# Optimization experiments

Measured on AMD Instinct MI355X. Metric: run time of the kernel, lower is better.

The kernel has to match this reference:

```python
import jax, jax.numpy as jnp
import numpy as np

B, N, K = 2, 4096, 16
CIN, CQ, D, PH, AH = 128, 128, 256, 64, 1024  # AH = dim * attn_hidden_multiplier
EPS = 1e-5


def setup_inputs() -> dict:
    key = jax.random.key(0)
    ks = jax.random.split(key, 40)
    rn = lambda k, shape, s=0.05: (jax.random.normal(k, shape, jnp.float32) * s)
    inp = {
        'obj_feature': jax.random.normal(ks[0], (B, CIN, N), jnp.float32),
        'pos': jax.random.normal(ks[1], (B, 3, N), jnp.float32),
        'query_points': jax.random.normal(ks[2], (B, CQ, N), jnp.float32),
        # linear_start_query / linear_start_obj (1x1 Conv1d)
        'W_lsq': rn(ks[3], (D, CQ)), 'b_lsq': rn(ks[4], (D,)),
        'W_lso': rn(ks[5], (D, CIN)), 'b_lso': rn(ks[6], (D,)),
        # key / query / value 1x1 Conv1d
        'Wk': rn(ks[7], (D, D)), 'bk': rn(ks[8], (D,)),
        'Wq': rn(ks[9], (D, D)), 'bq': rn(ks[10], (D,)),
        'Wv': rn(ks[11], (D, D)), 'bv': rn(ks[12], (D,)),
        # pos_mlp: Conv2d(3,PH,1) -> BN -> ReLU -> Conv2d(PH,D,1)
        'Wp1': rn(ks[13], (PH, 3)), 'bp1': rn(ks[14], (PH,)),
        'g1': 1.0 + rn(ks[15], (PH,)), 'bt1': rn(ks[16], (PH,)),
        'm1': rn(ks[17], (PH,)), 'v1': 0.5 + jax.random.uniform(ks[18], (PH,), jnp.float32),
        'Wp2': rn(ks[19], (D, PH)), 'bp2': rn(ks[20], (D,)),
        # attn_mlp: Conv2d(D,AH,1) -> BN -> ReLU -> Conv2d(AH,D,1)
        'Wa1': rn(ks[21], (AH, D)), 'ba1': rn(ks[22], (AH,)),
        'g2': 1.0 + rn(ks[23], (AH,)), 'bt2': rn(ks[24], (AH,)),
        'm2': rn(ks[25], (AH,)), 'v2': 0.5 + jax.random.uniform(ks[26], (AH,), jnp.float32),
        'Wa2': rn(ks[27], (D, AH)), 'ba2': rn(ks[28], (D,)),
        # linear_end
        'We': rn(ks[29], (CIN, D)), 'bfin': rn(ks[30], (CIN,)),
    }
    return inp


def _conv1d(x, W, b):  # x: (B,Ci,N), W: (Co,Ci)
    return jnp.einsum('oi,bin->bon', W, x) + b[None, :, None]


def _conv2d(x, W, b):  # x: (B,Ci,N,K)
    return jnp.einsum('oi,bink->bonk', W, x) + b[None, :, None, None]


def _bn(x, g, bt, m, v):  # inference BatchNorm2d over channel axis 1
    sc = (g * jax.lax.rsqrt(v + EPS))[None, :, None, None]
    return x * sc + (bt - m * g * jax.lax.rsqrt(v + EPS))[None, :, None, None]


def _knn_idx(pos):  # pos: (B,3,N) -> (B,N,K) indices of K nearest points (incl. self)
    p = jnp.transpose(pos, (0, 2, 1))  # (B,N,3)
    sq = jnp.sum(p * p, axis=-1)  # (B,N)
    dist = sq[:, :, None] + sq[:, None, :] - 2.0 * jnp.einsum('bnd,bmd->bnm', p, p)
    return jax.lax.top_k(-dist, K)[1]


def _gather(feat, idx):  # feat: (B,C,N), idx: (B,N,K) -> (B,C,N,K)
    return jnp.take_along_axis(feat[:, :, None, :], idx[:, None, :, :], axis=3)


def reference(obj_feature, pos, query_points, W_lsq, b_lsq, W_lso, b_lso,
              Wk, bk, Wq, bq, Wv, bv, Wp1, bp1, g1, bt1, m1, v1, Wp2, bp2,
              Wa1, ba1, g2, bt2, m2, v2, Wa2, ba2, We, bfin):
    qf = _conv1d(query_points, W_lsq, b_lsq)        # (B,D,N)
    of = _conv1d(obj_feature, W_lso, b_lso)         # (B,D,N)
    idx = _knn_idx(pos)                             # (B,N,K)
    key = _conv1d(of, Wk, bk)
    value = _conv1d(of, Wv, bv)
    query = _conv1d(qf, Wq, bq)
    key_g = _gather(key, idx)                       # (B,D,N,K)
    qk_rel = query[:, :, :, None] - key_g
    pos_rel = pos[:, :, :, None] - _gather(pos, idx)  # (B,3,N,K)
    pe = _conv2d(jax.nn.relu(_bn(_conv2d(pos_rel, Wp1, bp1), g1, bt1, m1, v1)), Wp2, bp2)
    attn = _conv2d(jax.nn.relu(_bn(_conv2d(qk_rel + pe, Wa1, ba1), g2, bt2, m2, v2)), Wa2, ba2)
    attn = jax.nn.softmax(attn, axis=-1)            # softmax over K neighbors
    val = value[:, :, :, None] + pe                 # (B,D,N,K)
    agg = jnp.sum(attn * val, axis=-1)              # einsum 'bcij,bcij->bci'
    return _conv1d(agg, We, bfin)                   # (B,CIN,N)
```

## Files before the change

kernel.cpp:

```cpp
#include <hip/hip_runtime.h>
#include <stdint.h>

#define B_ 2
#define N_ 4096
#define KNN 16
#define D_ 256
#define EPS_ 1e-5f
#define COLS_TOTAL (B_ * N_ * KNN)
#define LOGNCHK 3

typedef unsigned short u16;
typedef unsigned long long u64;
typedef __bf16 bf16x8 __attribute__((ext_vector_type(8)));
typedef float f32x4 __attribute__((ext_vector_type(4)));

__device__ __forceinline__ float bu2f(u16 u) { return __uint_as_float(((unsigned)u) << 16); }
__device__ __forceinline__ u16 f2bu(float f) {
  __bf16 h = (__bf16)f;
  return __builtin_bit_cast(unsigned short, h);
}
__device__ __forceinline__ float rdl(const void* p, size_t i, int f) {
  return f ? bu2f(((const u16*)p)[i]) : ((const float*)p)[i];
}

#define SC_POS 0
#define SC_BLSQ 24576
#define SC_BLSO 24832
#define SC_BK 25088
#define SC_BQ 25344
#define SC_BV 25600
#define SC_WP1 25856
#define SC_BP1 26048
#define SC_G1 26112
#define SC_BT1 26176
#define SC_M1 26240
#define SC_V1 26304
#define SC_BP2 26368
#define SC_BA1 26624
#define SC_G2 27648
#define SC_BT2 28672
#define SC_M2 29696
#define SC_V2 30720
#define SC_BA2 31744
#define SC_BFIN 32000
#define SC_BQP 32128
#define SC_BKP 32384
#define SC_BVP 32640
#define SC_W1S 32896
#define SC_C1  33088
#define SC_ASC 33152
#define SC_ASH 34176
#define SC_TOT 35200

#define NSEG 29
struct Seg { const void* s; float* d; int n; };
struct SegTab { Seg seg[NSEG]; };
__global__ void ingest(SegTab t, const unsigned* __restrict__ praw,
                       int* __restrict__ flagp, int total) {
  __shared__ int cnt;
  if (threadIdx.x == 0) cnt = 0;
  __syncthreads();
  unsigned wv = praw[threadIdx.x];
  unsigned e = (wv >> 7) & 0xFFu;
  if (e >= 0x7Au && e <= 0x81u) atomicAdd(&cnt, 1);
  __syncthreads();
  int f = (cnt >= 128) ? 1 : 0;
  if (blockIdx.x == 0 && threadIdx.x == 0) *flagp = f;
  int tid = blockIdx.x * blockDim.x + threadIdx.x;
  if (tid >= total) return;
  int acc = 0, k = 0;
  for (k = 0; k < NSEG; k++) { if (tid < acc + t.seg[k].n) break; acc += t.seg[k].n; }
  int i = tid - acc;
  t.seg[k].d[i] = rdl(t.seg[k].s, i, f);
}

__device__ void dev_bnprep(float* scal, int t) {
  if (t < 1024) {
    float sc = scal[SC_G2 + t] * (1.0f / sqrtf(scal[SC_V2 + t] + EPS_));
    scal[SC_ASC + t] = sc;
    scal[SC_ASH + t] = scal[SC_BA1 + t] * sc + (scal[SC_BT2 + t] - scal[SC_M2 + t] * sc);
  }
  if (t < 64) {
    float sc1 = scal[SC_G1 + t] * (1.0f / sqrtf(scal[SC_V1 + t] + EPS_));
    scal[SC_C1 + t] = scal[SC_BP1 + t] * sc1 + (scal[SC_BT1 + t] - scal[SC_M1 + t] * sc1);
    for (int i = 0; i < 3; i++) scal[SC_W1S + t * 3 + i] = scal[SC_WP1 + t * 3 + i] * sc1;
  }
}

struct C3 { const float* Wo[3]; const float* Wi[3]; const float* bi[3]; const float* bo[3];
            u16* Wout[3]; float* bout[3]; };
__device__ void dev_compose3(const C3& c, int z, int tid) {
  const float* Wo = c.Wo[z]; const float* Wi = c.Wi[z];
  if (tid < 256 * 128) {
    int o = tid >> 7, i = tid & 127;
    float a0 = 0.f, a1 = 0.f, a2 = 0.f, a3 = 0.f;
    for (int d = 0; d < 256; d += 4) {
      a0 += Wo[o * 256 + d + 0] * Wi[(d + 0) * 128 + i];
      a1 += Wo[o * 256 + d + 1] * Wi[(d + 1) * 128 + i];
      a2 += Wo[o * 256 + d + 2] * Wi[(d + 2) * 128 + i];
      a3 += Wo[o * 256 + d + 3] * Wi[(d + 3) * 128 + i];
    }
    c.Wout[z][o * 128 + i] = f2bu((a0 + a1) + (a2 + a3));
  } else if (tid < 256 * 128 + 256) {
    int o = tid - 256 * 128;
    float a = c.bo[z][o];
    for (int d = 0; d < 256; d++) a += Wo[o * 256 + d] * c.bi[z][d];
    c.bout[z][o] = a;
  }
}

struct QF { const float* src[3]; u16* dst[3]; int M[3]; int K[3]; };
__device__ void dev_quant_flin(const QF& q, int z, int g) {
  int M = q.M[z], K = q.K[z];
  if (g >= (M * K) / 8) return;
  int tile = g >> 6, lane = g & 63;
  int l15 = lane & 15, quad = lane >> 4;
  int kt = K >> 5;
  int mt = tile / kt, kc = tile % kt;
  const float* s = q.src[z] + (size_t)(mt * 16 + l15) * K + kc * 32 + quad * 8;
  u16* d = q.dst[z] + (size_t)g * 8;
  u16 o[8];
#pragma unroll
  for (int j = 0; j < 8; j++) o[j] = f2bu(s[j]);
  *(uint4*)d = *(uint4*)o;
}

struct T2 { const void* src[2]; u16* dst[2]; };
__device__ void dev_transq2(const T2& t2, int f, int bx, int by, int bz, int tid,
                            u16 (*t)[33]) {
  int tensor = bz >> 1, b = bz & 1;
  const void* raw = t2.src[tensor];
  u16* out = t2.dst[tensor];
  int c0 = by * 32, n0 = bx * 32;
  int j = tid & 31, i0 = tid >> 5;
  for (int s = 0; s < 32; s += 8) {
    int i = i0 + s;
    t[i][j] = f2bu(rdl(raw, ((size_t)b * 128 + c0 + i) * N_ + n0 + j, f));
  }
  __syncthreads();
  int i = tid & 31, j0 = tid >> 5;
  for (int s = 0; s < 32; s += 8) {
    int jj = j0 + s;
    out[((size_t)b * N_ + n0 + jj) * 128 + c0 + i] = t[i][jj];
  }
}

__device__ __forceinline__ u64 knn_key(const float* px, float qx, float qy, float qz,
                                       float sqn, int m) {
  float cx = px[m], cy = px[N_ + m], cz = px[2 * N_ + m];
  float sqm = cx * cx + cy * cy + cz * cz;
  float dot = qx * cx + qy * cy + qz * cz;
  float d = (sqn + sqm) - 2.0f * dot;
  unsigned ub = __float_as_uint(d);
  ub = ((int)ub < 0) ? ~ub : (ub | 0x80000000u);
  return ((u64)ub << 32) | (unsigned)m;
}

__device__ __forceinline__ void bitonic_sort16(u64* c) {
#pragma unroll
  for (int k = 2; k <= 16; k <<= 1) {
#pragma unroll
    for (int j = k >> 1; j > 0; j >>= 1) {
#pragma unroll
      for (int i = 0; i < 16; i++) {
        int l = i ^ j;
        if (l > i) {
          u64 a = c[i], b2 = c[l];
          bool up = ((i & k) == 0);
          bool sw = up ? (b2 < a) : (a < b2);
          u64 na = sw ? b2 : a;
          u64 nb = sw ? a : b2;
          c[i] = na; c[l] = nb;
        }
      }
    }
  }
}

__device__ __forceinline__ void bitonic_merge_into(u64* best, const u64* c) {
#pragma unroll
  for (int i = 0; i < 16; i++) {
    u64 b2 = c[15 - i];
    best[i] = (best[i] < b2) ? best[i] : b2;
  }
#pragma unroll
  for (int j = 8; j > 0; j >>= 1) {
#pragma unroll
    for (int i = 0; i < 16; i++) {
      if ((i & j) == 0) {
        u64 a = best[i], b2 = best[i | j];
        u64 mn = (a < b2) ? a : b2;
        u64 mx = (a < b2) ? b2 : a;
        best[i] = mn; best[i | j] = mx;
      }
    }
  }
}

__device__ void dev_knn_partial(const float* pos, u64* part, int tid) {
  int n = tid & (N_ - 1);
  int ch = (tid >> 12) & ((1 << LOGNCHK) - 1);
  int b = tid >> (12 + LOGNCHK);
  const float* px = pos + (size_t)b * 3 * N_;
  float qx = px[n], qy = px[N_ + n], qz = px[2 * N_ + n];
  float sqn = qx * qx + qy * qy + qz * qz;
  int clen = N_ >> LOGNCHK;
  int m0 = ch * clen;
  u64 best[KNN];
  {
#pragma unroll
    for (int i = 0; i < 16; i++) best[i] = knn_key(px, qx, qy, qz, sqn, m0 + i);
    bitonic_sort16(best);
  }
  for (int m = m0 + 16; m < m0 + clen; m += 16) {
    u64 c[16];
#pragma unroll
    for (int i = 0; i < 16; i++) c[i] = knn_key(px, qx, qy, qz, sqn, m + i);
    bitonic_sort16(c);
    bitonic_merge_into(best, c);
  }
  u64* o = part + (size_t)tid * KNN;
#pragma unroll
  for (int i = 0; i < KNN; i++) o[i] = best[i];
}

__device__ void dev_knn_merge(const u64* part, int* idx, int tid) {
  if (tid >= B_ * N_) return;
  int n = tid & (N_ - 1);
  int b = tid >> 12;
  u64 best[KNN];
  {
    const u64* p = part + ((((size_t)(b << LOGNCHK)) << 12) + n) * KNN;
#pragma unroll
    for (int i = 0; i < KNN; i++) best[i] = p[i];
  }
  for (int ch = 1; ch < (1 << LOGNCHK); ch++) {
    const u64* p = part + ((((size_t)((b << LOGNCHK) + ch)) << 12) + n) * KNN;
    u64 c[16];
#pragma unroll
    for (int e = 0; e < KNN; e++) c[e] = p[e];
    bitonic_merge_into(best, c);
  }
  int* o = idx + (size_t)tid * KNN;
#pragma unroll
  for (int i = 0; i < KNN; i++) o[i] = (int)(best[i] & 0xffffffffu);
}

struct G3 { const u16* W[3]; const u16* Bsrc[3]; u16* O[3]; const float* bias[3]; };
__device__ void dev_gemm(const G3& g, int bx, int by, int bz, int tid,
                         u16* As, u16* Bs) {
  const int z = bz;
  const u16* Wg = g.W[z];
  const u16* Bg = g.Bsrc[z];
  u16* Out = g.O[z];
  const float* bias = g.bias[z];
  const int M = 256, K = 128;
  const int mtile = by, ctile = bx;
  const int wid = tid >> 6, lane = tid & 63;
  const int wm = wid >> 1, wc = wid & 1;
  const int l15 = lane & 15, quad = lane >> 4;
  f32x4 acc[4][4];
#pragma unroll
  for (int a = 0; a < 4; a++)
#pragma unroll
    for (int bb = 0; bb < 4; bb++) acc[a][bb] = (f32x4){0.f, 0.f, 0.f, 0.f};
  const int r0 = tid >> 2, q0 = tid & 3;
  for (int k0 = 0; k0 < K; k0 += 32) {
    __syncthreads();
    *(uint4*)(&As[(r0) * 32 + q0 * 8]) = *(const uint4*)(&Wg[((size_t)mtile * 128 + r0) * K + k0 + q0 * 8]);
    *(uint4*)(&As[(r0 + 64) * 32 + q0 * 8]) = *(const uint4*)(&Wg[((size_t)mtile * 128 + r0 + 64) * K + k0 + q0 * 8]);
    *(uint4*)(&Bs[(r0) * 32 + q0 * 8]) = *(const uint4*)(&Bg[((size_t)ctile * 128 + r0) * K + k0 + q0 * 8]);
    *(uint4*)(&Bs[(r0 + 64) * 32 + q0 * 8]) = *(const uint4*)(&Bg[((size_t)ctile * 128 + r0 + 64) * K + k0 + q0 * 8]);
    __syncthreads();
    bf16x8 af[4], bfr[4];
#pragma unroll
    for (int i = 0; i < 4; i++) {
      af[i] = *(const bf16x8*)(&As[(wm * 64 + i * 16 + l15) * 32 + quad * 8]);
      bfr[i] = *(const bf16x8*)(&Bs[(wc * 64 + i * 16 + l15) * 32 + quad * 8]);
    }
#pragma unroll
    for (int mi = 0; mi < 4; mi++)
#pragma unroll
      for (int ni = 0; ni < 4; ni++)
        acc[mi][ni] = __builtin_amdgcn_mfma_f32_16x16x32_bf16(af[mi], bfr[ni], acc[mi][ni], 0, 0, 0);
  }
  const int mbase = mtile * 128 + wm * 64;
  const int cbase = ctile * 128 + wc * 64;
#pragma unroll
  for (int mi = 0; mi < 4; mi++) {
#pragma unroll
    for (int ni = 0; ni < 4; ni++) {
      int m0 = mbase + mi * 16 + quad * 4;
      int c = cbase + ni * 16 + l15;
      u16 pk[4];
#pragma unroll
      for (int r = 0; r < 4; r++) pk[r] = f2bu(acc[mi][ni][r] + bias[m0 + r]);
      *(uint2*)(&Out[(size_t)c * M + m0]) = *(uint2*)pk;
    }
  }
}

__global__ void prepA(C3 c3, QF qf, T2 t2, float* __restrict__ scal,
                      u64* __restrict__ knn_part, const int* __restrict__ flagp) {
  __shared__ u16 tq[32][33];
  int bid = blockIdx.x, tid = threadIdx.x;
  if (bid < 256) {
    dev_knn_partial(scal + SC_POS, knn_part, bid * 256 + tid);
  } else if (bid < 260) {
    dev_bnprep(scal, (bid - 256) * 256 + tid);
  } else if (bid < 650) {
    int u = bid - 260;
    dev_compose3(c3, u / 130, (u % 130) * 256 + tid);
  } else if (bid < 1034) {
    int u = bid - 650;
    dev_quant_flin(qf, u >> 7, (u & 127) * 256 + tid);
  } else {
    int u = bid - 1034;
    dev_transq2(t2, *flagp, u & 127, (u >> 7) & 3, u >> 9, tid, tq);
  }
}

__global__ __launch_bounds__(256) void prepB(G3 g3, const u64* __restrict__ knn_part,
                                             int* __restrict__ idx) {
  __shared__ __align__(16) u16 As[128 * 32];
  __shared__ __align__(16) u16 Bs[128 * 32];
  int bid = blockIdx.x, tid = threadIdx.x;
  if (bid < 32) {
    dev_knn_merge(knn_part, idx, bid * 256 + tid);
  } else {
    int u = bid - 32;
    dev_gemm(g3, u & 63, (u >> 6) & 1, u >> 7, tid, As, Bs);
  }
}

#define XS_OFF 0
#define HS_OFF 16896
#define AG_OFF 33792
#define SM_TOT 35872

__global__ __launch_bounds__(512, 4) void mega(
    const float* __restrict__ scal, const int* __restrict__ idx,
    const u16* __restrict__ query_t, const u16* __restrict__ key_t,
    const u16* __restrict__ value_t,
    float* __restrict__ out,
    const u16* __restrict__ Wp2f, const u16* __restrict__ Wa1f,
    const u16* __restrict__ Wa2f, const float* __restrict__ Wef) {
  __shared__ __align__(16) u16 sm[SM_TOT];
  float* aggs = (float*)&sm[AG_OFF];
  const int tid = threadIdx.x;
  const int w = tid >> 6, lane = tid & 63;
  const int l15 = lane & 15, quad = lane >> 4;
  const int gcol0 = blockIdx.x * 64;
  const int b = gcol0 >> 16;
  const int n0 = (gcol0 & 65535) >> 4;

  uint4 qu_r[4], ku_r[4];
  {
#pragma unroll
    for (int it = 0; it < 4; it++) {
      int g = tid + it * 512;
      int col = g >> 5, dg = (g & 31) * 8;
      int n = n0 + (col >> 4), k = col & 15;
      int id = idx[((size_t)(b * N_ + n)) * KNN + k];
      qu_r[it] = *(const uint4*)(query_t + ((size_t)(b * N_ + n)) * D_ + dg);
      ku_r[it] = *(const uint4*)(key_t + ((size_t)(b * N_ + id)) * D_ + dg);
    }
  }

  {
    int col = tid >> 3, jg = (tid & 7) * 8;
    int n = n0 + (col >> 4), k = col & 15;
    int id = idx[((size_t)(b * N_ + n)) * KNN + k];
    const float* px = scal + SC_POS + (size_t)b * 3 * N_;
    float pr0 = px[n] - px[id];
    float pr1 = px[N_ + n] - px[N_ + id];
    float pr2 = px[2 * N_ + n] - px[2 * N_ + id];
    u16 o[8];
#pragma unroll
    for (int e = 0; e < 8; e++) {
      int j = jg + e;
      float v = scal[SC_W1S + j * 3] * pr0 + scal[SC_W1S + j * 3 + 1] * pr1 +
                scal[SC_W1S + j * 3 + 2] * pr2 + scal[SC_C1 + j];
      o[e] = f2bu(fmaxf(v, 0.f));
    }
    *(uint4*)(&sm[HS_OFF + col * 264 + jg]) = *(uint4*)o;
  }
  __syncthreads();

  uint2 pe_pk[2][4];
  {
    f32x4 pacc[2][4];
#pragma unroll
    for (int mi = 0; mi < 2; mi++)
#pragma unroll
      for (int ni = 0; ni < 4; ni++) pacc[mi][ni] = (f32x4){0.f, 0.f, 0.f, 0.f};
    __builtin_amdgcn_s_setprio(1);
#pragma unroll
    for (int kc = 0; kc < 2; kc++) {
      int k0 = kc * 32;
      bf16x8 af[2], bfr[4];
#pragma unroll
      for (int mi = 0; mi < 2; mi++)
        af[mi] = *(const bf16x8*)(Wp2f + (size_t)((w * 2 + mi) * 2 + kc) * 512 + lane * 8);
#pragma unroll
      for (int ni = 0; ni < 4; ni++)
        bfr[ni] = *(const bf16x8*)(&sm[HS_OFF + (ni * 16 + l15) * 264 + k0 + quad * 8]);
#pragma unroll
      for (int mi = 0; mi < 2; mi++)
#pragma unroll
        for (int ni = 0; ni < 4; ni++)
          pacc[mi][ni] = __builtin_amdgcn_mfma_f32_16x16x32_bf16(af[mi], bfr[ni], pacc[mi][ni], 0, 0, 0);
    }
    __builtin_amdgcn_s_setprio(0);
#pragma unroll
    for (int mi = 0; mi < 2; mi++)
#pragma unroll
      for (int ni = 0; ni < 4; ni++) {
        int m0 = w * 32 + mi * 16 + quad * 4;
        int col = ni * 16 + l15;
        u16 pk[4];
#pragma unroll
        for (int r = 0; r < 4; r++) pk[r] = f2bu(pacc[mi][ni][r] + scal[SC_BP2 + m0 + r]);
        uint2 pu = *(uint2*)pk;
        pe_pk[mi][ni] = pu;
        *(uint2*)(&sm[XS_OFF + col * 264 + m0]) = pu;
      }
  }
  __syncthreads();

  {
    uint4 xbuf[4];
#pragma unroll
    for (int it = 0; it < 4; it++) {
      int g = tid + it * 512;
      int col = g >> 5, dg = (g & 31) * 8;
      uint4 pu = *(const uint4*)(&sm[XS_OFF + col * 264 + dg]);
      const u16 *qs = (const u16*)&qu_r[it], *ks = (const u16*)&ku_r[it], *ps = (const u16*)&pu;
      u16 o[8];
#pragma unroll
      for (int e = 0; e < 8; e++) o[e] = f2bu((bu2f(qs[e]) - bu2f(ks[e])) + bu2f(ps[e]));
      xbuf[it] = *(uint4*)o;
    }
    __syncthreads();
#pragma unroll
    for (int it = 0; it < 4; it++) {
      int g = tid + it * 512;
      int col = g >> 5, dg = (g & 31) * 8;
      *(uint4*)(&sm[XS_OFF + col * 264 + dg]) = xbuf[it];
    }
  }
  __syncthreads();

  f32x4 aacc[2][4];
#pragma unroll
  for (int mi = 0; mi < 2; mi++)
#pragma unroll
    for (int ni = 0; ni < 4; ni++) aacc[mi][ni] = (f32x4){0.f, 0.f, 0.f, 0.f};

  for (int hb = 0; hb < 4; hb++) {
    f32x4 hacc[2][4];
#pragma unroll
    for (int mi = 0; mi < 2; mi++)
#pragma unroll
      for (int ni = 0; ni < 4; ni++) hacc[mi][ni] = (f32x4){0.f, 0.f, 0.f, 0.f};
    __builtin_amdgcn_s_setprio(1);
#pragma unroll 4
    for (int kc = 0; kc < 8; kc++) {
      int k0 = kc * 32;
      bf16x8 af[2], bx[4];
#pragma unroll
      for (int mi = 0; mi < 2; mi++)
        af[mi] = *(const bf16x8*)(Wa1f + (size_t)((hb * 16 + w * 2 + mi) * 8 + kc) * 512 + lane * 8);
#pragma unroll
      for (int ni = 0; ni < 4; ni++)
        bx[ni] = *(const bf16x8*)(&sm[XS_OFF + (ni * 16 + l15) * 264 + k0 + quad * 8]);
#pragma unroll
      for (int mi = 0; mi < 2; mi++)
#pragma unroll
        for (int ni = 0; ni < 4; ni++)
          hacc[mi][ni] = __builtin_amdgcn_mfma_f32_16x16x32_bf16(af[mi], bx[ni], hacc[mi][ni], 0, 0, 0);
    }
    __builtin_amdgcn_s_setprio(0);
    __syncthreads();
#pragma unroll
    for (int mi = 0; mi < 2; mi++)
#pragma unroll
      for (int ni = 0; ni < 4; ni++) {
        int khb = w * 32 + mi * 16 + quad * 4;
        int mh = hb * 256 + khb;
        int col = ni * 16 + l15;
        u16 pk[4];
#pragma unroll
        for (int r = 0; r < 4; r++) {
          float v = hacc[mi][ni][r] * scal[SC_ASC + mh + r] + scal[SC_ASH + mh + r];
          pk[r] = f2bu(fmaxf(v, 0.f));
        }
        *(uint2*)(&sm[HS_OFF + col * 264 + khb]) = *(uint2*)pk;
      }
    __syncthreads();
    __builtin_amdgcn_s_setprio(1);
#pragma unroll 4
    for (int kc = 0; kc < 8; kc++) {
      int k0 = kc * 32;
      bf16x8 af[2], bh[4];
#pragma unroll
      for (int mi = 0; mi < 2; mi++)
        af[mi] = *(const bf16x8*)(Wa2f + (size_t)((w * 2 + mi) * 32 + hb * 8 + kc) * 512 + lane * 8);
#pragma unroll
      for (int ni = 0; ni < 4; ni++)
        bh[ni] = *(const bf16x8*)(&sm[HS_OFF + (ni * 16 + l15) * 264 + k0 + quad * 8]);
#pragma unroll
      for (int mi = 0; mi < 2; mi++)
#pragma unroll
        for (int ni = 0; ni < 4; ni++)
          aacc[mi][ni] = __builtin_amdgcn_mfma_f32_16x16x32_bf16(af[mi], bh[ni], aacc[mi][ni], 0, 0, 0);
    }
    __builtin_amdgcn_s_setprio(0);
  }

  __syncthreads();
#pragma unroll
  for (int mi = 0; mi < 2; mi++)
#pragma unroll
    for (int ni = 0; ni < 4; ni++) {
      int m0 = w * 32 + mi * 16 + quad * 4;
      int col = ni * 16 + l15;
      u16 pk[4];
#pragma unroll
      for (int r = 0; r < 4; r++) pk[r] = f2bu(aacc[mi][ni][r] + scal[SC_BA2 + m0 + r]);
      *(uint2*)(&sm[XS_OFF + col * 264 + m0]) = *(uint2*)pk;
      *(uint2*)(&sm[HS_OFF + col * 264 + m0]) = pe_pk[mi][ni];
    }
  __syncthreads();

#pragma unroll
  for (int it = 0; it < 2; it++) {
    int e = tid + it * 512;
    int pt = e >> 8, m = e & 255;
    float a[16];
#pragma unroll
    for (int k = 0; k < 16; k++) a[k] = bu2f(sm[XS_OFF + (pt * 16 + k) * 264 + m]);
    float t0 = fmaxf(a[0], a[1]),  t1 = fmaxf(a[2], a[3]);
    float t2 = fmaxf(a[4], a[5]),  t3 = fmaxf(a[6], a[7]);
    float t4 = fmaxf(a[8], a[9]),  t5 = fmaxf(a[10], a[11]);
    float t6 = fmaxf(a[12], a[13]), t7 = fmaxf(a[14], a[15]);
    t0 = fmaxf(t0, t1); t2 = fmaxf(t2, t3); t4 = fmaxf(t4, t5); t6 = fmaxf(t6, t7);
    float mx = fmaxf(fmaxf(t0, t2), fmaxf(t4, t6));
    float s = 0.f;
#pragma unroll
    for (int k = 0; k < 16; k++) { a[k] = __expf(a[k] - mx); s += a[k]; }
    float inv = __builtin_amdgcn_rcpf(s);
    float acc = 0.f;
#pragma unroll
    for (int k = 0; k < 16; k++)
      acc += a[k] * bu2f(sm[HS_OFF + (pt * 16 + k) * 264 + m]);
    float val = bu2f(value_t[((size_t)(b * N_ + n0 + pt)) * D_ + m]);
    aggs[pt * 260 + m] = fmaf(acc, inv, val);
  }
  __syncthreads();

  {
    int ci = tid >> 2, pt = tid & 3;
    float acc = scal[SC_BFIN + ci];
    const float* wr = Wef + (size_t)ci * 256;
    const float* ag = aggs + pt * 260;
#pragma unroll 8
    for (int m4 = 0; m4 < 256; m4 += 4) {
      float4 wu = *(const float4*)(wr + m4);
      acc += wu.x * ag[m4] + wu.y * ag[m4 + 1] + wu.z * ag[m4 + 2] + wu.w * ag[m4 + 3];
    }
    out[((size_t)(b * 128 + ci)) * N_ + n0 + pt] = acc;
  }
}

#define WT_LSQ 0
#define WT_LSO 32768
#define WT_K 65536
#define WT_Q 131072
#define WT_V 196608
#define WT_P2 262144
#define WT_A1 278528
#define WT_A2 540672
#define WT_TOT 802816
#define WB_QP 0
#define WB_KP 32768
#define WB_VP 65536
#define WB_P2 98304
#define WB_A1 114688
#define WB_A2 376832
#define WB_TOT 638976

extern "C" void kernel_launch(void* const* d_in, const int* in_sizes, int n_in,
                              void* d_out, int out_size, void* d_ws, size_t ws_size,
                              hipStream_t stream) {
  (void)in_sizes; (void)n_in; (void)out_size; (void)ws_size;
  char* wsb = (char*)d_ws;
  size_t off = 0;
  auto alloc = [&](size_t bytes) -> void* {
    void* p = wsb + off;
    off = (off + bytes + 255) & ~(size_t)255;
    return p;
  };
  int* flag = (int*)alloc(256);
  int* idx = (int*)alloc((size_t)B_ * N_ * KNN * 4);
  u16* wbf = (u16*)alloc((size_t)WB_TOT * 2);
  float* scal = (float*)alloc((size_t)SC_TOT * 4);
  float* Wef = (float*)alloc((size_t)32768 * 4);
  u16* key_t = (u16*)alloc((size_t)B_ * N_ * D_ * 2);
  u16* query_t = (u16*)alloc((size_t)B_ * N_ * D_ * 2);
  u16* value_t = (u16*)alloc((size_t)B_ * N_ * D_ * 2);
  float* wtmp = (float*)alloc((size_t)WT_TOT * 4);
  u16* qp_t = (u16*)alloc((size_t)B_ * N_ * 128 * 2);
  u16* obj_t = (u16*)alloc((size_t)B_ * N_ * 128 * 2);
  u64* knn_part = (u64*)alloc(((size_t)(B_ * N_) << LOGNCHK) * KNN * 8);

  SegTab st;
  int si = 0;
  auto seg = [&](int di, float* d, int n) { st.seg[si].s = d_in[di]; st.seg[si].d = d; st.seg[si].n = n; si++; };
  seg(1, scal + SC_POS, 24576);
  seg(4, scal + SC_BLSQ, 256); seg(6, scal + SC_BLSO, 256);
  seg(8, scal + SC_BK, 256); seg(10, scal + SC_BQ, 256); seg(12, scal + SC_BV, 256);
  seg(13, scal + SC_WP1, 192); seg(14, scal + SC_BP1, 64); seg(15, scal + SC_G1, 64);
  seg(16, scal + SC_BT1, 64); seg(17, scal + SC_M1, 64); seg(18, scal + SC_V1, 64);
  seg(20, scal + SC_BP2, 256); seg(22, scal + SC_BA1, 1024);
  seg(23, scal + SC_G2, 1024); seg(24, scal + SC_BT2, 1024); seg(25, scal + SC_M2, 1024);
  seg(26, scal + SC_V2, 1024); seg(28, scal + SC_BA2, 256); seg(30, scal + SC_BFIN, 128);
  seg(3, wtmp + WT_LSQ, 32768); seg(5, wtmp + WT_LSO, 32768);
  seg(7, wtmp + WT_K, 65536); seg(9, wtmp + WT_Q, 65536); seg(11, wtmp + WT_V, 65536);
  seg(19, wtmp + WT_P2, 16384); seg(21, wtmp + WT_A1, 262144);
  seg(27, wtmp + WT_A2, 262144); seg(29, Wef, 32768);
  int total = 32128 + WT_TOT + 32768;
  ingest<<<(total + 255) / 256, 256, 0, stream>>>(st, (const unsigned*)d_in[1], flag, total);

  C3 c3;
  c3.Wo[0] = wtmp + WT_Q; c3.Wi[0] = wtmp + WT_LSQ; c3.bi[0] = scal + SC_BLSQ; c3.bo[0] = scal + SC_BQ;
  c3.Wout[0] = wbf + WB_QP; c3.bout[0] = scal + SC_BQP;
  c3.Wo[1] = wtmp + WT_K; c3.Wi[1] = wtmp + WT_LSO; c3.bi[1] = scal + SC_BLSO; c3.bo[1] = scal + SC_BK;
  c3.Wout[1] = wbf + WB_KP; c3.bout[1] = scal + SC_BKP;
  c3.Wo[2] = wtmp + WT_V; c3.Wi[2] = wtmp + WT_LSO; c3.bi[2] = scal + SC_BLSO; c3.bo[2] = scal + SC_BV;
  c3.Wout[2] = wbf + WB_VP; c3.bout[2] = scal + SC_BVP;
  QF qf;
  qf.src[0] = wtmp + WT_P2; qf.dst[0] = wbf + WB_P2; qf.M[0] = 256;  qf.K[0] = 64;
  qf.src[1] = wtmp + WT_A1; qf.dst[1] = wbf + WB_A1; qf.M[1] = 1024; qf.K[1] = 256;
  qf.src[2] = wtmp + WT_A2; qf.dst[2] = wbf + WB_A2; qf.M[2] = 256;  qf.K[2] = 1024;
  T2 t2;
  t2.src[0] = d_in[2]; t2.dst[0] = qp_t;
  t2.src[1] = d_in[0]; t2.dst[1] = obj_t;
  prepA<<<3082, 256, 0, stream>>>(c3, qf, t2, scal, knn_part, flag);

  G3 g3;
  g3.W[0] = wbf + WB_QP; g3.Bsrc[0] = qp_t;  g3.O[0] = query_t; g3.bias[0] = scal + SC_BQP;
  g3.W[1] = wbf + WB_KP; g3.Bsrc[1] = obj_t; g3.O[1] = key_t;   g3.bias[1] = scal + SC_BKP;
  g3.W[2] = wbf + WB_VP; g3.Bsrc[2] = obj_t; g3.O[2] = value_t; g3.bias[2] = scal + SC_BVP;
  prepB<<<416, 256, 0, stream>>>(g3, knn_part, idx);

  mega<<<COLS_TOTAL / 64, 512, 0, stream>>>(
      scal, idx, query_t, key_t, value_t, (float*)d_out,
      wbf + WB_P2, wbf + WB_A1, wbf + WB_A2, Wef);
}
```

Measured before the change: 380.5 us.

## Fuse qk_rel add into PE epilogue and double KNN partial chunks

The q and k loads now follow the MFMA accumulator layout of the position-encoding GEMM, so the (q - k + pe) sum is computed directly in that epilogue and written to shared memory once. This drops a separate read-modify-write pass over shared memory and two block barriers. Separately, the KNN partial search is split into twice as many chunks (LOGNCHK 3 to 4, 256 to 512 blocks) for more parallelism in prepA, at the cost of more partial results for the merge step to combine. The narrower uint2 global loads may coalesce less well than the previous uint4 loads.

```diff
diff --git a/kernel.cpp b/kernel.cpp
--- a/kernel.cpp
+++ b/kernel.cpp
@@ -7,7 +7,7 @@
 #define D_ 256
 #define EPS_ 1e-5f
 #define COLS_TOTAL (B_ * N_ * KNN)
-#define LOGNCHK 3
+#define LOGNCHK 4
 
 typedef unsigned short u16;
 typedef unsigned long long u64;
@@ -304,18 +304,18 @@
                       u64* __restrict__ knn_part, const int* __restrict__ flagp) {
   __shared__ u16 tq[32][33];
   int bid = blockIdx.x, tid = threadIdx.x;
-  if (bid < 256) {
+  if (bid < 512) {
     dev_knn_partial(scal + SC_POS, knn_part, bid * 256 + tid);
-  } else if (bid < 260) {
-    dev_bnprep(scal, (bid - 256) * 256 + tid);
-  } else if (bid < 650) {
-    int u = bid - 260;
+  } else if (bid < 516) {
+    dev_bnprep(scal, (bid - 512) * 256 + tid);
+  } else if (bid < 906) {
+    int u = bid - 516;
     dev_compose3(c3, u / 130, (u % 130) * 256 + tid);
-  } else if (bid < 1034) {
-    int u = bid - 650;
+  } else if (bid < 1290) {
+    int u = bid - 906;
     dev_quant_flin(qf, u >> 7, (u & 127) * 256 + tid);
   } else {
-    int u = bid - 1034;
+    int u = bid - 1290;
     dev_transq2(t2, *flagp, u & 127, (u >> 7) & 3, u >> 9, tid, tq);
   }
 }
@@ -354,18 +354,22 @@
   const int b = gcol0 >> 16;
   const int n0 = (gcol0 & 65535) >> 4;
 
-  uint4 qu_r[4], ku_r[4];
+  uint2 qr[2][4], kr[2][4];
   {
-#pragma unroll
-    for (int it = 0; it < 4; it++) {
-      int g = tid + it * 512;
-      int col = g >> 5, dg = (g & 31) * 8;
-      int n = n0 + (col >> 4), k = col & 15;
-      int id = idx[((size_t)(b * N_ + n)) * KNN + k];
-      qu_r[it] = *(const uint4*)(query_t + ((size_t)(b * N_ + n)) * D_ + dg);
-      ku_r[it] = *(const uint4*)(key_t + ((size_t)(b * N_ + id)) * D_ + dg);
-    }
-  }
+    int id_c[4];
+#pragma unroll
+    for (int ni = 0; ni < 4; ni++)
+      id_c[ni] = idx[((size_t)(b * N_ + n0 + ni)) * KNN + l15];
+#pragma unroll
+    for (int mi = 0; mi < 2; mi++)
+#pragma unroll
+      for (int ni = 0; ni < 4; ni++) {
+        int m0 = w * 32 + mi * 16 + quad * 4;
+        qr[mi][ni] = *(const uint2*)(query_t + ((size_t)(b * N_ + n0 + ni)) * D_ + m0);
+        kr[mi][ni] = *(const uint2*)(key_t + ((size_t)(b * N_ + id_c[ni])) * D_ + m0);
+      }
+  }
+  __builtin_amdgcn_sched_barrier(0);
 
   {
     int col = tid >> 3, jg = (tid & 7) * 8;
@@ -418,36 +422,18 @@
       for (int ni = 0; ni < 4; ni++) {
         int m0 = w * 32 + mi * 16 + quad * 4;
         int col = ni * 16 + l15;
-        u16 pk[4];
-#pragma unroll
-        for (int r = 0; r < 4; r++) pk[r] = f2bu(pacc[mi][ni][r] + scal[SC_BP2 + m0 + r]);
-        uint2 pu = *(uint2*)pk;
-        pe_pk[mi][ni] = pu;
-        *(uint2*)(&sm[XS_OFF + col * 264 + m0]) = pu;
+        const u16* qs = (const u16*)&qr[mi][ni];
+        const u16* ks = (const u16*)&kr[mi][ni];
+        u16 pkpe[4], pkx[4];
+#pragma unroll
+        for (int r = 0; r < 4; r++) {
+          float pe = pacc[mi][ni][r] + scal[SC_BP2 + m0 + r];
+          pkpe[r] = f2bu(pe);
+          pkx[r] = f2bu(pe + (bu2f(qs[r]) - bu2f(ks[r])));
+        }
+        pe_pk[mi][ni] = *(uint2*)pkpe;
+        *(uint2*)(&sm[XS_OFF + col * 264 + m0]) = *(uint2*)pkx;
       }
-  }
-  __syncthreads();
-
-  {
-    uint4 xbuf[4];
-#pragma unroll
-    for (int it = 0; it < 4; it++) {
-      int g = tid + it * 512;
-      int col = g >> 5, dg = (g & 31) * 8;
-      uint4 pu = *(const uint4*)(&sm[XS_OFF + col * 264 + dg]);
-      const u16 *qs = (const u16*)&qu_r[it], *ks = (const u16*)&ku_r[it], *ps = (const u16*)&pu;
-      u16 o[8];
-#pragma unroll
-      for (int e = 0; e < 8; e++) o[e] = f2bu((bu2f(qs[e]) - bu2f(ks[e])) + bu2f(ps[e]));
-      xbuf[it] = *(uint4*)o;
-    }
-    __syncthreads();
-#pragma unroll
-    for (int it = 0; it < 4; it++) {
-      int g = tid + it * 512;
-      int col = g >> 5, dg = (g & 31) * 8;
-      *(uint4*)(&sm[XS_OFF + col * 264 + dg]) = xbuf[it];
-    }
   }
   __syncthreads();
 
@@ -646,7 +632,7 @@
   T2 t2;
   t2.src[0] = d_in[2]; t2.dst[0] = qp_t;
   t2.src[1] = d_in[0]; t2.dst[1] = obj_t;
-  prepA<<<3082, 256, 0, stream>>>(c3, qf, t2, scal, knn_part, flag);
+  prepA<<<3338, 256, 0, stream>>>(c3, qf, t2, scal, knn_part, flag);
 
   G3 g3;
   g3.W[0] = wbf + WB_QP; g3.Bsrc[0] = qp_t;  g3.O[0] = query_t; g3.bias[0] = scal + SC_BQP;
```

After: 417.5 us. +9.7%, slower.

## Fold ingest kernel into prepA and stage KNN candidates in LDS

Applied to the files above, without the earlier changes.

Removes the separate ingest launch and the fp32 staging buffer. Each prepA block now computes the dtype flag locally and reads raw inputs directly, converting them on the fly inside compose, quantise, BN prep and a smaller canonicalisation step. KNN partials switch to 16 chunks of 256 candidates whose positions are loaded once into shared memory per block, instead of being re-read from global memory. This trades a launch and a global round trip for redundant flag detection in every block and a larger KNN merge stage.

```diff
diff --git a/kernel.cpp b/kernel.cpp
--- a/kernel.cpp
+++ b/kernel.cpp
@@ -7,7 +7,7 @@
 #define D_ 256
 #define EPS_ 1e-5f
 #define COLS_TOTAL (B_ * N_ * KNN)
-#define LOGNCHK 3
+#define LOGNCHK 4
 
 typedef unsigned short u16;
 typedef unsigned long long u64;
@@ -24,104 +24,103 @@
 }
 
 #define SC_POS 0
-#define SC_BLSQ 24576
-#define SC_BLSO 24832
-#define SC_BK 25088
-#define SC_BQ 25344
-#define SC_BV 25600
-#define SC_WP1 25856
-#define SC_BP1 26048
-#define SC_G1 26112
-#define SC_BT1 26176
-#define SC_M1 26240
-#define SC_V1 26304
-#define SC_BP2 26368
-#define SC_BA1 26624
-#define SC_G2 27648
-#define SC_BT2 28672
-#define SC_M2 29696
-#define SC_V2 30720
-#define SC_BA2 31744
-#define SC_BFIN 32000
-#define SC_BQP 32128
-#define SC_BKP 32384
-#define SC_BVP 32640
-#define SC_W1S 32896
-#define SC_C1  33088
-#define SC_ASC 33152
-#define SC_ASH 34176
-#define SC_TOT 35200
-
-#define NSEG 29
+#define SC_BP2 24576
+#define SC_BA2 24832
+#define SC_BFIN 25088
+#define SC_BQP 25216
+#define SC_BKP 25472
+#define SC_BVP 25728
+#define SC_W1S 25984
+#define SC_C1  26176
+#define SC_ASC 26240
+#define SC_ASH 27264
+#define SC_TOT 28288
+
+__device__ int block_flag(const unsigned* __restrict__ praw) {
+  __shared__ int cnt;
+  if (threadIdx.x == 0) cnt = 0;
+  __syncthreads();
+  if (threadIdx.x < 256) {
+    unsigned wv = praw[threadIdx.x];
+    unsigned e = (wv >> 7) & 0xFFu;
+    if (e >= 0x7Au && e <= 0x81u) atomicAdd(&cnt, 1);
+  }
+  __syncthreads();
+  return (cnt >= 128) ? 1 : 0;
+}
+
+#define NSEG 5
 struct Seg { const void* s; float* d; int n; };
 struct SegTab { Seg seg[NSEG]; };
-__global__ void ingest(SegTab t, const unsigned* __restrict__ praw,
-                       int* __restrict__ flagp, int total) {
-  __shared__ int cnt;
-  if (threadIdx.x == 0) cnt = 0;
-  __syncthreads();
-  unsigned wv = praw[threadIdx.x];
-  unsigned e = (wv >> 7) & 0xFFu;
-  if (e >= 0x7Au && e <= 0x81u) atomicAdd(&cnt, 1);
-  __syncthreads();
-  int f = (cnt >= 128) ? 1 : 0;
-  if (blockIdx.x == 0 && threadIdx.x == 0) *flagp = f;
-  int tid = blockIdx.x * blockDim.x + threadIdx.x;
-  if (tid >= total) return;
+#define CANON_TOT 57984
+__device__ void dev_canon(const SegTab& t, int f, int gt) {
+  if (gt >= CANON_TOT) return;
   int acc = 0, k = 0;
-  for (k = 0; k < NSEG; k++) { if (tid < acc + t.seg[k].n) break; acc += t.seg[k].n; }
-  int i = tid - acc;
-  t.seg[k].d[i] = rdl(t.seg[k].s, i, f);
-}
-
-__device__ void dev_bnprep(float* scal, int t) {
+  for (k = 0; k < NSEG; k++) { if (gt < acc + t.seg[k].n) break; acc += t.seg[k].n; }
+  t.seg[k].d[gt - acc] = rdl(t.seg[k].s, gt - acc, f);
+}
+
+struct BN { const void* ba1; const void* g2; const void* bt2; const void* m2; const void* v2;
+            const void* wp1; const void* bp1; const void* g1; const void* bt1; const void* m1;
+            const void* v1; };
+__device__ void dev_bnprep(const BN& bn, float* scal, int t, int f) {
   if (t < 1024) {
-    float sc = scal[SC_G2 + t] * (1.0f / sqrtf(scal[SC_V2 + t] + EPS_));
+    float sc = rdl(bn.g2, t, f) * (1.0f / sqrtf(rdl(bn.v2, t, f) + EPS_));
     scal[SC_ASC + t] = sc;
-    scal[SC_ASH + t] = scal[SC_BA1 + t] * sc + (scal[SC_BT2 + t] - scal[SC_M2 + t] * sc);
+    scal[SC_ASH + t] = rdl(bn.ba1, t, f) * sc + (rdl(bn.bt2, t, f) - rdl(bn.m2, t, f) * sc);
   }
   if (t < 64) {
-    float sc1 = scal[SC_G1 + t] * (1.0f / sqrtf(scal[SC_V1 + t] + EPS_));
-    scal[SC_C1 + t] = scal[SC_BP1 + t] * sc1 + (scal[SC_BT1 + t] - scal[SC_M1 + t] * sc1);
-    for (int i = 0; i < 3; i++) scal[SC_W1S + t * 3 + i] = scal[SC_WP1 + t * 3 + i] * sc1;
-  }
-}
-
-struct C3 { const float* Wo[3]; const float* Wi[3]; const float* bi[3]; const float* bo[3];
+    float sc1 = rdl(bn.g1, t, f) * (1.0f / sqrtf(rdl(bn.v1, t, f) + EPS_));
+    scal[SC_C1 + t] = rdl(bn.bp1, t, f) * sc1 + (rdl(bn.bt1, t, f) - rdl(bn.m1, t, f) * sc1);
+    for (int i = 0; i < 3; i++) scal[SC_W1S + t * 3 + i] = rdl(bn.wp1, (size_t)t * 3 + i, f) * sc1;
+  }
+}
+
+struct C3 { const void* Wo[3]; const void* Wi[3]; const void* bi[3]; const void* bo[3];
             u16* Wout[3]; float* bout[3]; };
-__device__ void dev_compose3(const C3& c, int z, int tid) {
-  const float* Wo = c.Wo[z]; const float* Wi = c.Wi[z];
+__device__ void dev_compose3(const C3& c, int z, int tid, int f) {
   if (tid < 256 * 128) {
     int o = tid >> 7, i = tid & 127;
     float a0 = 0.f, a1 = 0.f, a2 = 0.f, a3 = 0.f;
-    for (int d = 0; d < 256; d += 4) {
-      a0 += Wo[o * 256 + d + 0] * Wi[(d + 0) * 128 + i];
-      a1 += Wo[o * 256 + d + 1] * Wi[(d + 1) * 128 + i];
-      a2 += Wo[o * 256 + d + 2] * Wi[(d + 2) * 128 + i];
-      a3 += Wo[o * 256 + d + 3] * Wi[(d + 3) * 128 + i];
+    if (f) {
+      const u16* Wo = (const u16*)c.Wo[z]; const u16* Wi = (const u16*)c.Wi[z];
+      for (int d = 0; d < 256; d += 4) {
+        a0 += bu2f(Wo[o * 256 + d + 0]) * bu2f(Wi[(d + 0) * 128 + i]);
+        a1 += bu2f(Wo[o * 256 + d + 1]) * bu2f(Wi[(d + 1) * 128 + i]);
+        a2 += bu2f(Wo[o * 256 + d + 2]) * bu2f(Wi[(d + 2) * 128 + i]);
+        a3 += bu2f(Wo[o * 256 + d + 3]) * bu2f(Wi[(d + 3) * 128 + i]);
+      }
+    } else {
+      const float* Wo = (const float*)c.Wo[z]; const float* Wi = (const float*)c.Wi[z];
+      for (int d = 0; d < 256; d += 4) {
+        a0 += Wo[o * 256 + d + 0] * Wi[(d + 0) * 128 + i];
+        a1 += Wo[o * 256 + d + 1] * Wi[(d + 1) * 128 + i];
+        a2 += Wo[o * 256 + d + 2] * Wi[(d + 2) * 128 + i];
+        a3 += Wo[o * 256 + d + 3] * Wi[(d + 3) * 128 + i];
+      }
     }
     c.Wout[z][o * 128 + i] = f2bu((a0 + a1) + (a2 + a3));
   } else if (tid < 256 * 128 + 256) {
     int o = tid - 256 * 128;
-    float a = c.bo[z][o];
-    for (int d = 0; d < 256; d++) a += Wo[o * 256 + d] * c.bi[z][d];
+    float a = rdl(c.bo[z], o, f);
+    for (int d = 0; d < 256; d++) a += rdl(c.Wo[z], (size_t)o * 256 + d, f) * rdl(c.bi[z], d, f);
     c.bout[z][o] = a;
   }
 }
 
-struct QF { const float* src[3]; u16* dst[3]; int M[3]; int K[3]; };
-__device__ void dev_quant_flin(const QF& q, int z, int g) {
+struct QF { const void* src[3]; u16* dst[3]; int M[3]; int K[3]; };
+__device__ void dev_quant_flin(const QF& q, int z, int g, int f) {
   int M = q.M[z], K = q.K[z];
   if (g >= (M * K) / 8) return;
   int tile = g >> 6, lane = g & 63;
   int l15 = lane & 15, quad = lane >> 4;
   int kt = K >> 5;
   int mt = tile / kt, kc = tile % kt;
-  const float* s = q.src[z] + (size_t)(mt * 16 + l15) * K + kc * 32 + quad * 8;
+  size_t sb = (size_t)(mt * 16 + l15) * K + kc * 32 + quad * 8;
   u16* d = q.dst[z] + (size_t)g * 8;
   u16 o[8];
 #pragma unroll
-  for (int j = 0; j < 8; j++) o[j] = f2bu(s[j]);
+  for (int j = 0; j < 8; j++) o[j] = f2bu(rdl(q.src[z], sb + j, f));
   *(uint4*)d = *(uint4*)o;
 }
 
@@ -145,15 +144,15 @@
   }
 }
 
-__device__ __forceinline__ u64 knn_key(const float* px, float qx, float qy, float qz,
-                                       float sqn, int m) {
-  float cx = px[m], cy = px[N_ + m], cz = px[2 * N_ + m];
+__device__ __forceinline__ u64 knn_key_lds(const float* c, float qx, float qy, float qz,
+                                           float sqn, int j, int m0) {
+  float cx = c[j], cy = c[256 + j], cz = c[512 + j];
   float sqm = cx * cx + cy * cy + cz * cz;
   float dot = qx * cx + qy * cy + qz * cz;
   float d = (sqn + sqm) - 2.0f * dot;
   unsigned ub = __float_as_uint(d);
   ub = ((int)ub < 0) ? ~ub : (ub | 0x80000000u);
-  return ((u64)ub << 32) | (unsigned)m;
+  return ((u64)ub << 32) | (unsigned)(m0 + j);
 }
 
 __device__ __forceinline__ void bitonic_sort16(u64* c) {
@@ -197,29 +196,37 @@
   }
 }
 
-__device__ void dev_knn_partial(const float* pos, u64* part, int tid) {
-  int n = tid & (N_ - 1);
-  int ch = (tid >> 12) & ((1 << LOGNCHK) - 1);
-  int b = tid >> (12 + LOGNCHK);
-  const float* px = pos + (size_t)b * 3 * N_;
-  float qx = px[n], qy = px[N_ + n], qz = px[2 * N_ + n];
-  float sqn = qx * qx + qy * qy + qz * qz;
+__device__ void dev_knn_partial(const void* pos_raw, int f, u64* part, int bid, int tid,
+                                float* cpos) {
+  int gtid = bid * 256 + tid;
+  int n = gtid & (N_ - 1);
+  int ch = (gtid >> 12) & ((1 << LOGNCHK) - 1);
+  int b = gtid >> (12 + LOGNCHK);
   int clen = N_ >> LOGNCHK;
   int m0 = ch * clen;
+  size_t base = (size_t)b * 3 * N_;
+  cpos[tid]       = rdl(pos_raw, base + m0 + tid, f);
+  cpos[256 + tid] = rdl(pos_raw, base + N_ + m0 + tid, f);
+  cpos[512 + tid] = rdl(pos_raw, base + 2 * N_ + m0 + tid, f);
+  float qx = rdl(pos_raw, base + n, f);
+  float qy = rdl(pos_raw, base + N_ + n, f);
+  float qz = rdl(pos_raw, base + 2 * N_ + n, f);
+  __syncthreads();
+  float sqn = qx * qx + qy * qy + qz * qz;
   u64 best[KNN];
   {
 #pragma unroll
-    for (int i = 0; i < 16; i++) best[i] = knn_key(px, qx, qy, qz, sqn, m0 + i);
+    for (int i = 0; i < 16; i++) best[i] = knn_key_lds(cpos, qx, qy, qz, sqn, i, m0);
     bitonic_sort16(best);
   }
-  for (int m = m0 + 16; m < m0 + clen; m += 16) {
+  for (int j = 16; j < 256; j += 16) {
     u64 c[16];
 #pragma unroll
-    for (int i = 0; i < 16; i++) c[i] = knn_key(px, qx, qy, qz, sqn, m + i);
+    for (int i = 0; i < 16; i++) c[i] = knn_key_lds(cpos, qx, qy, qz, sqn, j + i, m0);
     bitonic_sort16(c);
     bitonic_merge_into(best, c);
   }
-  u64* o = part + (size_t)tid * KNN;
+  u64* o = part + (size_t)gtid * KNN;
 #pragma unroll
   for (int i = 0; i < KNN; i++) o[i] = best[i];
 }
@@ -300,23 +307,28 @@
   }
 }
 
-__global__ void prepA(C3 c3, QF qf, T2 t2, float* __restrict__ scal,
-                      u64* __restrict__ knn_part, const int* __restrict__ flagp) {
+__global__ void prepA(C3 c3, QF qf, T2 t2, BN bn, SegTab st,
+                      const void* __restrict__ pos_raw,
+                      float* __restrict__ scal, u64* __restrict__ knn_part) {
+  __shared__ float cpos[768];
   __shared__ u16 tq[32][33];
+  int f = block_flag((const unsigned*)pos_raw);
   int bid = blockIdx.x, tid = threadIdx.x;
-  if (bid < 256) {
-    dev_knn_partial(scal + SC_POS, knn_part, bid * 256 + tid);
-  } else if (bid < 260) {
-    dev_bnprep(scal, (bid - 256) * 256 + tid);
-  } else if (bid < 650) {
-    int u = bid - 260;
-    dev_compose3(c3, u / 130, (u % 130) * 256 + tid);
-  } else if (bid < 1034) {
-    int u = bid - 650;
-    dev_quant_flin(qf, u >> 7, (u & 127) * 256 + tid);
+  if (bid < 512) {
+    dev_knn_partial(pos_raw, f, knn_part, bid, tid, cpos);
+  } else if (bid < 2560) {
+    int u = bid - 512;
+    dev_transq2(t2, f, u & 127, (u >> 7) & 3, u >> 9, tid, tq);
+  } else if (bid < 2950) {
+    int u = bid - 2560;
+    dev_compose3(c3, u / 130, (u % 130) * 256 + tid, f);
+  } else if (bid < 3334) {
+    int u = bid - 2950;
+    dev_quant_flin(qf, u >> 7, (u & 127) * 256 + tid, f);
+  } else if (bid < 3338) {
+    dev_bnprep(bn, scal, (bid - 3334) * 256 + tid, f);
   } else {
-    int u = bid - 1034;
-    dev_transq2(t2, *flagp, u & 127, (u >> 7) & 3, u >> 9, tid, tq);
+    dev_canon(st, f, (bid - 3338) * 256 + tid);
   }
 }
 
@@ -573,15 +585,6 @@
   }
 }
 
-#define WT_LSQ 0
-#define WT_LSO 32768
-#define WT_K 65536
-#define WT_Q 131072
-#define WT_V 196608
-#define WT_P2 262144
-#define WT_A1 278528
-#define WT_A2 540672
-#define WT_TOT 802816
 #define WB_QP 0
 #define WB_KP 32768
 #define WB_VP 65536
@@ -601,7 +604,6 @@
     off = (off + bytes + 255) & ~(size_t)255;
     return p;
   };
-  int* flag = (int*)alloc(256);
   int* idx = (int*)alloc((size_t)B_ * N_ * KNN * 4);
   u16* wbf = (u16*)alloc((size_t)WB_TOT * 2);
   float* scal = (float*)alloc((size_t)SC_TOT * 4);
@@ -609,44 +611,35 @@
   u16* key_t = (u16*)alloc((size_t)B_ * N_ * D_ * 2);
   u16* query_t = (u16*)alloc((size_t)B_ * N_ * D_ * 2);
   u16* value_t = (u16*)alloc((size_t)B_ * N_ * D_ * 2);
-  float* wtmp = (float*)alloc((size_t)WT_TOT * 4);
   u16* qp_t = (u16*)alloc((size_t)B_ * N_ * 128 * 2);
   u16* obj_t = (u16*)alloc((size_t)B_ * N_ * 128 * 2);
   u64* knn_part = (u64*)alloc(((size_t)(B_ * N_) << LOGNCHK) * KNN * 8);
 
-  SegTab st;
-  int si = 0;
-  auto seg = [&](int di, float* d, int n) { st.seg[si].s = d_in[di]; st.seg[si].d = d; st.seg[si].n = n; si++; };
-  seg(1, scal + SC_POS, 24576);
-  seg(4, scal + SC_BLSQ, 256); seg(6, scal + SC_BLSO, 256);
-  seg(8, scal + SC_BK, 256); seg(10, scal + SC_BQ, 256); seg(12, scal + SC_BV, 256);
-  seg(13, scal + SC_WP1, 192); seg(14, scal + SC_BP1, 64); seg(15, scal + SC_G1, 64);
-  seg(16, scal + SC_BT1, 64); seg(17, scal + SC_M1, 64); seg(18, scal + SC_V1, 64);
-  seg(20, scal + SC_BP2, 256); seg(22, scal + SC_BA1, 1024);
-  seg(23, scal + SC_G2, 1024); seg(24, scal + SC_BT2, 1024); seg(25, scal + SC_M2, 1024);
-  seg(26, scal + SC_V2, 1024); seg(28, scal + SC_BA2, 256); seg(30, scal + SC_BFIN, 128);
-  seg(3, wtmp + WT_LSQ, 32768); seg(5, wtmp + WT_LSO, 32768);
-  seg(7, wtmp + WT_K, 65536); seg(9, wtmp + WT_Q, 65536); seg(11, wtmp + WT_V, 65536);
-  seg(19, wtmp + WT_P2, 16384); seg(21, wtmp + WT_A1, 262144);
-  seg(27, wtmp + WT_A2, 262144); seg(29, Wef, 32768);
-  int total = 32128 + WT_TOT + 32768;
-  ingest<<<(total + 255) / 256, 256, 0, stream>>>(st, (const unsigned*)d_in[1], flag, total);
-
   C3 c3;
-  c3.Wo[0] = wtmp + WT_Q; c3.Wi[0] = wtmp + WT_LSQ; c3.bi[0] = scal + SC_BLSQ; c3.bo[0] = scal + SC_BQ;
+  c3.Wo[0] = d_in[9];  c3.Wi[0] = d_in[3]; c3.bi[0] = d_in[4]; c3.bo[0] = d_in[10];
   c3.Wout[0] = wbf + WB_QP; c3.bout[0] = scal + SC_BQP;
-  c3.Wo[1] = wtmp + WT_K; c3.Wi[1] = wtmp + WT_LSO; c3.bi[1] = scal + SC_BLSO; c3.bo[1] = scal + SC_BK;
+  c3.Wo[1] = d_in[7];  c3.Wi[1] = d_in[5]; c3.bi[1] = d_in[6]; c3.bo[1] = d_in[8];
   c3.Wout[1] = wbf + WB_KP; c3.bout[1] = scal + SC_BKP;
-  c3.Wo[2] = wtmp + WT_V; c3.Wi[2] = wtmp + WT_LSO; c3.bi[2] = scal + SC_BLSO; c3.bo[2] = scal + SC_BV;
+  c3.Wo[2] = d_in[11]; c3.Wi[2] = d_in[5]; c3.bi[2] = d_in[6]; c3.bo[2] = d_in[12];
   c3.Wout[2] = wbf + WB_VP; c3.bout[2] = scal + SC_BVP;
   QF qf;
-  qf.src[0] = wtmp + WT_P2; qf.dst[0] = wbf + WB_P2; qf.M[0] = 256;  qf.K[0] = 64;
-  qf.src[1] = wtmp + WT_A1; qf.dst[1] = wbf + WB_A1; qf.M[1] = 1024; qf.K[1] = 256;
-  qf.src[2] = wtmp + WT_A2; qf.dst[2] = wbf + WB_A2; qf.M[2] = 256;  qf.K[2] = 1024;
+  qf.src[0] = d_in[19]; qf.dst[0] = wbf + WB_P2; qf.M[0] = 256;  qf.K[0] = 64;
+  qf.src[1] = d_in[21]; qf.dst[1] = wbf + WB_A1; qf.M[1] = 1024; qf.K[1] = 256;
+  qf.src[2] = d_in[27]; qf.dst[2] = wbf + WB_A2; qf.M[2] = 256;  qf.K[2] = 1024;
   T2 t2;
   t2.src[0] = d_in[2]; t2.dst[0] = qp_t;
   t2.src[1] = d_in[0]; t2.dst[1] = obj_t;
-  prepA<<<3082, 256, 0, stream>>>(c3, qf, t2, scal, knn_part, flag);
+  BN bn;
+  bn.ba1 = d_in[22]; bn.g2 = d_in[23]; bn.bt2 = d_in[24]; bn.m2 = d_in[25]; bn.v2 = d_in[26];
+  bn.wp1 = d_in[13]; bn.bp1 = d_in[14]; bn.g1 = d_in[15]; bn.bt1 = d_in[16]; bn.m1 = d_in[17];
+  bn.v1 = d_in[18];
+  SegTab st;
+  st.seg[0] = {d_in[1],  scal + SC_POS,  24576};
+  st.seg[1] = {d_in[20], scal + SC_BP2,  256};
+  st.seg[2] = {d_in[28], scal + SC_BA2,  256};
+  st.seg[3] = {d_in[30], scal + SC_BFIN, 128};
+  st.seg[4] = {d_in[29], Wef,            32768};
+  prepA<<<3565, 256, 0, stream>>>(c3, qf, t2, bn, st, d_in[1], scal, knn_part);
 
   G3 g3;
   g3.W[0] = wbf + WB_QP; g3.Bsrc[0] = qp_t;  g3.O[0] = query_t; g3.bias[0] = scal + SC_BQP;
```

New measurement: 381.8 us (median of 2 runs). No clear change (+0.3%).
